# Optimization experiments

Hardware: AMD Instinct MI355X
Metric: run time of the kernel (lower is better)

## Reference

```python
import jax, jax.numpy as jnp
import numpy as np

B, C, H, W = 4, 64, 224, 224
WS = 14
HEADS = 4
HD = C // HEADS  # 16
N = WS * WS      # 196
SCALE = HD ** -0.5


def conv2d(x, w, b, pad):
    y = jax.lax.conv_general_dilated(x, w, (1, 1), [(pad, pad), (pad, pad)],
                                     dimension_numbers=('NCHW', 'OIHW', 'NCHW'))
    return y + b[None, :, None, None]


def layernorm(x, g, b, eps=1e-5):
    m = jnp.mean(x, axis=-1, keepdims=True)
    v = jnp.mean((x - m) ** 2, axis=-1, keepdims=True)
    return (x - m) * jax.lax.rsqrt(v + eps) * g + b


def window_partition(x):
    # x: (B,H,W,C) -> (B*nW, WS, WS, C)
    b, h, w, c = x.shape
    x = x.reshape(b, h // WS, WS, w // WS, WS, c)
    return x.transpose(0, 1, 3, 2, 4, 5).reshape(-1, WS, WS, c)


def window_reverse(win, h, w):
    b = win.shape[0] // ((h // WS) * (w // WS))
    x = win.reshape(b, h // WS, w // WS, WS, WS, -1)
    return x.transpose(0, 1, 3, 2, 4, 5).reshape(b, h, w, -1)


def setup_inputs():
    key = jax.random.key(0)
    ks = iter(jax.random.split(key, 64))
    nrm = lambda shp, s=0.02: (jax.random.normal(next(ks), shp, jnp.float32) * s)
    d = {}
    d['x'] = jax.random.normal(next(ks), (B, C, H, W), jnp.float32)
    d['x_basic'] = jax.random.normal(next(ks), (B, C, H, W), jnp.float32)
    # Aware_offset convs
    d['c1_w'] = nrm((64, 64, 3, 3)); d['c1_b'] = jnp.zeros((64,), jnp.float32)
    d['c2_w'] = nrm((64, 64, 5, 5)); d['c2_b'] = jnp.zeros((64,), jnp.float32)
    d['c3_w'] = nrm((64, 64, 7, 7)); d['c3_b'] = jnp.zeros((64,), jnp.float32)
    d['c4_w'] = nrm((64, 192, 3, 3)); d['c4_b'] = jnp.zeros((64,), jnp.float32)
    d['c5_w'] = nrm((128, 128, 3, 3)); d['c5_b'] = jnp.zeros((128,), jnp.float32)
    d['c6_w'] = nrm((128, 128, 3, 3)); d['c6_b'] = jnp.zeros((128,), jnp.float32)
    d['c7_w'] = nrm((64, 128, 1, 1)); d['c7_b'] = jnp.zeros((64,), jnp.float32)
    d['c8_w'] = nrm((64, 128, 1, 1)); d['c8_b'] = jnp.zeros((64,), jnp.float32)
    # block params
    d['qkv1_w'] = nrm((64, 64, 3, 3)); d['qkv1_b'] = jnp.zeros((64,), jnp.float32)
    d['n1_g'] = jnp.ones((C,), jnp.float32); d['n1_b'] = jnp.zeros((C,), jnp.float32)
    d['qkv_w'] = nrm((3 * C, C)); d['qkv_b'] = jnp.zeros((3 * C,), jnp.float32)
    d['corr_w'] = nrm((N, HD)); d['corr_b'] = jnp.zeros((N,), jnp.float32)
    d['proj_w'] = nrm((C, C)); d['proj_b'] = jnp.zeros((C,), jnp.float32)
    d['n2_g'] = jnp.ones((C,), jnp.float32); d['n2_b'] = jnp.zeros((C,), jnp.float32)
    d['fc1_w'] = nrm((2 * C, C)); d['fc1_b'] = jnp.zeros((2 * C,), jnp.float32)
    d['fc2_w'] = nrm((C, 2 * C)); d['fc2_b'] = jnp.zeros((C,), jnp.float32)
    return d


def _forward(x, x_basic, c1_w, c1_b, c2_w, c2_b, c3_w, c3_b, c4_w, c4_b,
             c5_w, c5_b, c6_w, c6_b, c7_w, c7_b, c8_w, c8_b,
             qkv1_w, qkv1_b, n1_g, n1_b, qkv_w, qkv_b, corr_w, corr_b,
             proj_w, proj_b, n2_g, n2_b, fc1_w, fc1_b, fc2_w, fc2_b):
    relu = jax.nn.relu
    # ---- Aware_offset ----
    in1 = relu(conv2d(x, c1_w, c1_b, 1))
    in2 = relu(conv2d(x, c2_w, c2_b, 2))
    in3 = relu(conv2d(x, c3_w, c3_b, 3))
    xo = relu(conv2d(jnp.concatenate([in1, in2, in3], 1), c4_w, c4_b, 1))
    cat12 = jnp.concatenate([x, x_basic], 1)
    b1 = relu(conv2d(cat12, c5_w, c5_b, 1))
    b2 = jax.nn.sigmoid(relu(conv2d(b1, c6_w, c6_b, 1)))
    b1 = relu(conv2d(b1 * b2, c7_w, c7_b, 0))
    xb = xo * b1 + relu(conv2d(cat12, c8_w, c8_b, 0))  # (B,C,H,W)
    xb = xb.transpose(0, 2, 3, 1)                       # (B,H,W,C)
    # ---- pre-attn: norm1 + convQKV1 ----
    xt = x.reshape(B, C, H * W).transpose(0, 2, 1)      # (B,L,C)
    xt = layernorm(xt, n1_g, n1_b)
    xc = xt.reshape(B, H, W, C).transpose(0, 3, 1, 2)
    xc = conv2d(xc, qkv1_w, qkv1_b, 1).transpose(0, 2, 3, 1)  # (B,H,W,C)
    # ---- windows ----
    xw = window_partition(xc).reshape(-1, N, C)   # (B_,N,C)
    xbw = window_partition(xb).reshape(-1, N, C)
    B_ = xw.shape[0]
    # ---- window attention with correction bias ----
    qkv = (xw @ qkv_w.T + qkv_b).reshape(B_, N, 3, HEADS, HD).transpose(2, 0, 3, 1, 4)
    q, k, v = qkv[0] * SCALE, qkv[1], qkv[2]            # (B_,h,N,hd)
    xcorr = xbw.reshape(B_, N, HEADS, HD).transpose(0, 2, 1, 3)
    xcorr = xcorr @ corr_w.T + corr_b                   # (B_,h,N,196)
    attn = jax.nn.softmax(jnp.einsum('bhnd,bhmd->bhnm', q, k) + xcorr, axis=-1)
    out = jnp.einsum('bhnm,bhmd->bhnd', attn, v).transpose(0, 2, 1, 3).reshape(B_, N, C)
    out = out @ proj_w.T + proj_b
    # ---- reverse + MLP ----
    sx = window_reverse(out.reshape(-1, WS, WS, C), H, W)  # (B,H,W,C)
    xt = sx.reshape(B, H * W, C)
    h = layernorm(xt, n2_g, n2_b)
    h = jax.nn.gelu(h @ fc1_w.T + fc1_b, approximate=False) @ fc2_w.T + fc2_b
    xt = xt + h
    return xt.reshape(B, H, W, C).transpose(0, 3, 1, 2)


def reference(x, x_basic, c1_w, c1_b, c2_w, c2_b, c3_w, c3_b, c4_w, c4_b,
              c5_w, c5_b, c6_w, c6_b, c7_w, c7_b, c8_w, c8_b,
              qkv1_w, qkv1_b, n1_g, n1_b, qkv_w, qkv_b, corr_w, corr_b,
              proj_w, proj_b, n2_g, n2_b, fc1_w, fc1_b, fc2_w, fc2_b):
    return _forward(x, x_basic, c1_w, c1_b, c2_w, c2_b, c3_w, c3_b, c4_w, c4_b,
                    c5_w, c5_b, c6_w, c6_b, c7_w, c7_b, c8_w, c8_b,
                    qkv1_w, qkv1_b, n1_g, n1_b, qkv_w, qkv_b, corr_w, corr_b,
                    proj_w, proj_b, n2_g, n2_b, fc1_w, fc1_b, fc2_w, fc2_b)
```

## Files before the change

### kernel.cpp

```cpp
#include <hip/hip_runtime.h>
#include <hip/hip_bf16.h>
#include <math.h>


#define HW  50176
#define WID 224

typedef unsigned short ushortT;
typedef __attribute__((ext_vector_type(8))) short bf8_t;
typedef __attribute__((ext_vector_type(4))) short bf4_t;
typedef __attribute__((ext_vector_type(4))) float f4_t;

__device__ __forceinline__ ushortT f2bf(float v) {
    __hip_bfloat16 h = __float2bfloat16(v);
    ushortT u; __builtin_memcpy(&u, &h, 2); return u;
}
__device__ __forceinline__ float bf2f(ushortT h) {
    union { float f; unsigned int u; } c; c.u = ((unsigned int)h) << 16;
    return c.f;
}
__device__ __forceinline__ void cvt8(const float* xv, bf8_t& hh, bf8_t& ll) {
    #pragma unroll
    for (int i = 0; i < 8; ++i) {
        ushortT hi = f2bf(xv[i]);
        hh[i] = (short)hi;
        ll[i] = (short)f2bf(xv[i] - bf2f(hi));
    }
}

__global__ __launch_bounds__(256) void packw(
    const float* __restrict__ w, ushortT* __restrict__ dst,
    int K, int IC, int OC, int total)
{
    int e = blockIdx.x * 256 + threadIdx.x;
    if (e >= total) return;
    int KK = K * K;
    int kk = e % KK; int rem = e / KK;
    int ic = rem % IC; int oc = rem / IC;
    float v = w[e];
    ushortT hi = f2bf(v);
    ushortT lo = f2bf(v - bf2f(hi));
    int g = oc >> 6, oc64 = oc & 63;
    int ic32 = ic >> 5, icin = ic & 31, kb = icin >> 3, ii = icin & 7;
    int nch = KK * (IC / 32);
    int chunk = ic32 * KK + kk;
    size_t base = ((size_t)(g * nch + chunk)) * 4096;
    dst[base + (kb * 64 + oc64) * 8 + ii] = hi;
    dst[base + 2048 + (kb * 64 + oc64) * 8 + ii] = lo;
}

__global__ __launch_bounds__(256) void packa32(
    const float* __restrict__ w, ushortT* __restrict__ dst, int K, int total)
{
    int e = blockIdx.x * 256 + threadIdx.x;
    if (e >= total) return;
    int f = e >> 9, r = e & 511, ln = r >> 3, i = r & 7;
    int nk = K >> 5;
    int o = f / nk, ks = f % nk;
    int c = ln & 15, gg = ln >> 4;
    float v = w[(size_t)(o * 16 + c) * K + ks * 32 + gg * 8 + i];
    ushortT hi = f2bf(v);
    dst[(size_t)f * 1024 + ln * 8 + i] = hi;
    dst[(size_t)f * 1024 + 512 + ln * 8 + i] = f2bf(v - bf2f(hi));
}

__global__ __launch_bounds__(256) void packa16(
    const float* __restrict__ w, ushortT* __restrict__ dst, int K, int total)
{
    int e = blockIdx.x * 256 + threadIdx.x;
    if (e >= total) return;
    int f = e >> 8, r = e & 255, ln = r >> 2, i = r & 3;
    int nk = K >> 4;
    int o = f / nk, n = f % nk;
    int c = ln & 15, gg = ln >> 4;
    float v = w[(size_t)(o * 16 + c) * K + n * 16 + gg * 4 + i];
    ushortT hi = f2bf(v);
    dst[(size_t)f * 512 + ln * 4 + i] = hi;
    dst[(size_t)f * 512 + 256 + ln * 4 + i] = f2bf(v - bf2f(hi));
}

template<int K>
__device__ __forceinline__ void convpass(
    const ushortT* __restrict__ wq, const ushortT* __restrict__ sm,
    int wv, int lc, int kb, f4_t (&ac)[2][4])
{
    constexpr int off = 3 - K / 2;
    constexpr int INSH = 14 * 22 * 40;
    constexpr int KK = K * K;
    const int boff = (kb * 64 + lc) * 8;

    bf8_t bA[4], lA[4], bB[4], lB[4];
    #pragma unroll
    for (int n = 0; n < 4; ++n) {
        bA[n] = *(const bf8_t*)(wq + boff + n * 128);
        lA[n] = *(const bf8_t*)(wq + 2048 + boff + n * 128);
    }
    auto domfma = [&](int kk, bf8_t (&bh)[4], bf8_t (&bl)[4]) {
        const int ky = kk / K, kx = kk % K;
        #pragma unroll
        for (int m = 0; m < 2; ++m) {
            const int row = 2 * wv + m + ky + off;
            const int col = lc + kx + off;
            const ushortT* ab = sm + (row * 22 + col) * 40 + kb * 8;
            bf8_t Ah = *(const bf8_t*)ab;
            bf8_t Al = *(const bf8_t*)(ab + INSH);
            #pragma unroll
            for (int n = 0; n < 4; ++n) {
                ac[m][n] = __builtin_amdgcn_mfma_f32_16x16x32_bf16(Ah, bh[n], ac[m][n], 0, 0, 0);
                ac[m][n] = __builtin_amdgcn_mfma_f32_16x16x32_bf16(Ah, bl[n], ac[m][n], 0, 0, 0);
                ac[m][n] = __builtin_amdgcn_mfma_f32_16x16x32_bf16(Al, bh[n], ac[m][n], 0, 0, 0);
            }
        }
    };
    #pragma unroll 1
    for (int kk = 0; kk + 2 <= KK; kk += 2) {
        const ushortT* w1 = wq + (size_t)(kk + 1) * 4096;
        #pragma unroll
        for (int n = 0; n < 4; ++n) {
            bB[n] = *(const bf8_t*)(w1 + boff + n * 128);
            lB[n] = *(const bf8_t*)(w1 + 2048 + boff + n * 128);
        }
        domfma(kk, bA, lA);
        const ushortT* w2 = wq + (size_t)(kk + 2) * 4096;
        #pragma unroll
        for (int n = 0; n < 4; ++n) {
            bA[n] = *(const bf8_t*)(w2 + boff + n * 128);
            lA[n] = *(const bf8_t*)(w2 + 2048 + boff + n * 128);
        }
        domfma(kk + 1, bB, lB);
    }
    domfma(KK - 1, bA, lA);
}

__global__ __launch_bounds__(256, 4) void mfconv3(
    const float* __restrict__ in,
    const ushortT* __restrict__ w1p, const ushortT* __restrict__ w2p,
    const ushortT* __restrict__ w3p,
    const float* __restrict__ b1, const float* __restrict__ b2,
    const float* __restrict__ b3,
    float* __restrict__ out, int inStride, int outStride)
{
    constexpr int TWd = 22, THd = 14, ICP = 40;
    constexpr int INSH = THd * TWd * ICP;
    constexpr int E = THd * TWd * 32;
    __shared__ __align__(16) ushortT smem_u[2 * INSH];

    const int t = threadIdx.x, lane = t & 63, wv = t >> 6;
    const int lc = lane & 15, kb = lane >> 4;
    const int img = blockIdx.z;
    const int x0 = blockIdx.x * 16, y0 = blockIdx.y * 8;
    const float* inb = in + (size_t)img * inStride;

    f4_t acc1[2][4], acc2[2][4], acc3[2][4];
    {
        #pragma unroll
        for (int n = 0; n < 4; ++n) {
            float z1 = b1[n * 16 + lc], z2 = b2[n * 16 + lc], z3 = b3[n * 16 + lc];
            #pragma unroll
            for (int m = 0; m < 2; ++m) {
                acc1[m][n] = (f4_t){z1, z1, z1, z1};
                acc2[m][n] = (f4_t){z2, z2, z2, z2};
                acc3[m][n] = (f4_t){z3, z3, z3, z3};
            }
        }
    }

    #pragma unroll 1
    for (int ic32 = 0; ic32 < 2; ++ic32) {
        __syncthreads();
        #pragma unroll 1
        for (int ib = 0; ib < E; ib += 2048) {
            float v[8];
            #pragma unroll
            for (int u = 0; u < 8; ++u) {
                int i = ib + u * 256 + t;
                v[u] = 0.f;
                if (i < E) {
                    int icn = i / (THd * TWd);
                    int px  = i % (THd * TWd);
                    int ty = px / TWd, tx = px % TWd;
                    int gy = y0 + ty - 3, gx = x0 + tx - 3;
                    if (gy >= 0 && gy < WID && gx >= 0 && gx < WID)
                        v[u] = inb[(size_t)(ic32 * 32 + icn) * HW + gy * WID + gx];
                }
            }
            #pragma unroll
            for (int u = 0; u < 8; ++u) {
                int i = ib + u * 256 + t;
                if (i < E) {
                    int icn = i / (THd * TWd);
                    int px  = i % (THd * TWd);
                    ushortT hi = f2bf(v[u]);
                    smem_u[px * ICP + icn] = hi;
                    smem_u[INSH + px * ICP + icn] = f2bf(v[u] - bf2f(hi));
                }
            }
        }
        __syncthreads();
        convpass<3>(w1p + (size_t)(ic32 *  9) * 4096, smem_u, wv, lc, kb, acc1);
        convpass<5>(w2p + (size_t)(ic32 * 25) * 4096, smem_u, wv, lc, kb, acc2);
        convpass<7>(w3p + (size_t)(ic32 * 49) * 4096, smem_u, wv, lc, kb, acc3);
    }

    #pragma unroll
    for (int c = 0; c < 3; ++c) {
        float* ob0 = out + (size_t)img * outStride + (size_t)(c * 64) * HW;
        #pragma unroll
        for (int m = 0; m < 2; ++m) {
            const int y = y0 + 2 * wv + m;
            #pragma unroll
            for (int n = 0; n < 4; ++n) {
                f4_t v = (c == 0) ? acc1[m][n] : (c == 1) ? acc2[m][n] : acc3[m][n];
                float4 st = { fmaxf(v[0], 0.f), fmaxf(v[1], 0.f),
                              fmaxf(v[2], 0.f), fmaxf(v[3], 0.f) };
                *(float4*)&ob0[(size_t)(n * 16 + lc) * HW + (size_t)y * WID + x0 + kb * 4] = st;
            }
        }
    }
}

template<int K, int IC, int OC, int ACT, bool CAT, bool LNRM, bool NHWCOUT>
__global__ __launch_bounds__(256, 4) void mfconv(
    const float* __restrict__ in, const float* __restrict__ in2,
    const ushortT* __restrict__ wpk, const float* __restrict__ bias,
    const float* __restrict__ mu, const float* __restrict__ rs,
    const float* __restrict__ lng, const float* __restrict__ lnb,
    float* __restrict__ out, int inStride, int outStride)
{
    constexpr int P = K / 2, TWd = 16 + K - 1, THd = 8 + K - 1, ICP = 40;
    constexpr int OCG = OC / 64, KK = K * K, NCH = KK * (IC / 32);
    constexpr int INSH = THd * TWd * ICP;
    constexpr int E = THd * TWd * 32;
    constexpr int SMU = (2 * INSH > 10240) ? 2 * INSH : 10240;
    __shared__ __align__(16) ushortT smem_u[SMU];
    float* pool = (float*)smem_u;

    const int t = threadIdx.x, lane = t & 63, wv = t >> 6;
    const int lc = lane & 15, kb = lane >> 4;
    const int img = blockIdx.z / OCG, g = blockIdx.z % OCG;
    const int x0 = blockIdx.x * 16, y0 = blockIdx.y * 8;
    const float* inb  = in + (size_t)img * inStride;
    const float* in2b = CAT ? (in2 + (size_t)img * inStride) : nullptr;
    const int imgPixBase = img * HW;
    const ushortT* wq0 = wpk + (size_t)g * NCH * 4096;

    f4_t acc[2][4];
    {
        float bz0 = bias[g * 64 +  0 + lc];
        float bz1 = bias[g * 64 + 16 + lc];
        float bz2 = bias[g * 64 + 32 + lc];
        float bz3 = bias[g * 64 + 48 + lc];
        #pragma unroll
        for (int m = 0; m < 2; ++m) {
            acc[m][0] = (f4_t){bz0, bz0, bz0, bz0};
            acc[m][1] = (f4_t){bz1, bz1, bz1, bz1};
            acc[m][2] = (f4_t){bz2, bz2, bz2, bz2};
            acc[m][3] = (f4_t){bz3, bz3, bz3, bz3};
        }
    }
    const int aoff = lc * ICP + kb * 8;
    const int boff = (kb * 64 + lc) * 8;

    #pragma unroll 1
    for (int ic32 = 0; ic32 < IC / 32; ++ic32) {
        __syncthreads();
        #pragma unroll 1
        for (int ib = 0; ib < E; ib += 2048) {
            float v[8];
            #pragma unroll
            for (int u = 0; u < 8; ++u) {
                int i = ib + u * 256 + t;
                v[u] = 0.f;
                if (i < E) {
                    int icn = i / (THd * TWd);
                    int px  = i % (THd * TWd);
                    int ty = px / TWd, tx = px % TWd;
                    int gy = y0 + ty - P, gx = x0 + tx - P;
                    int ic = ic32 * 32 + icn;
                    if (gy >= 0 && gy < WID && gx >= 0 && gx < WID) {
                        const float* s;
                        if (CAT) s = (ic < 64) ? (inb + (size_t)ic * HW)
                                               : (in2b + (size_t)(ic - 64) * HW);
                        else     s = inb + (size_t)ic * HW;
                        float vv = s[gy * WID + gx];
                        if (LNRM) {
                            int p = imgPixBase + gy * WID + gx;
                            vv = (vv - mu[p]) * rs[p] * lng[ic] + lnb[ic];
                        }
                        v[u] = vv;
                    }
                }
            }
            #pragma unroll
            for (int u = 0; u < 8; ++u) {
                int i = ib + u * 256 + t;
                if (i < E) {
                    int icn = i / (THd * TWd);
                    int px  = i % (THd * TWd);
                    ushortT hi = f2bf(v[u]);
                    smem_u[px * ICP + icn] = hi;
                    smem_u[INSH + px * ICP + icn] = f2bf(v[u] - bf2f(hi));
                }
            }
        }
        __syncthreads();
        const ushortT* wqb = wq0 + (size_t)(ic32 * KK) * 4096;
        bf8_t bA[4], lA[4], bB[4], lB[4];
        #pragma unroll
        for (int n = 0; n < 4; ++n) {
            bA[n] = *(const bf8_t*)(wqb + boff + n * 128);
            lA[n] = *(const bf8_t*)(wqb + 2048 + boff + n * 128);
        }
        auto domfma = [&](int kk, bf8_t (&bh)[4], bf8_t (&bl)[4]) {
            const int ky = kk / K, kx = kk % K;
            #pragma unroll
            for (int m = 0; m < 2; ++m) {
                const int row = 2 * wv + m + ky;
                const ushortT* ab = smem_u + (row * TWd + kx) * ICP + aoff;
                bf8_t Ah = *(const bf8_t*)ab;
                bf8_t Al = *(const bf8_t*)(ab + INSH);
                #pragma unroll
                for (int n = 0; n < 4; ++n) {
                    acc[m][n] = __builtin_amdgcn_mfma_f32_16x16x32_bf16(Ah, bh[n], acc[m][n], 0, 0, 0);
                    acc[m][n] = __builtin_amdgcn_mfma_f32_16x16x32_bf16(Ah, bl[n], acc[m][n], 0, 0, 0);
                    acc[m][n] = __builtin_amdgcn_mfma_f32_16x16x32_bf16(Al, bh[n], acc[m][n], 0, 0, 0);
                }
            }
        };
        #pragma unroll 1
        for (int kk = 0; kk + 2 <= KK; kk += 2) {
            const ushortT* w1 = wqb + (size_t)(kk + 1) * 4096;
            #pragma unroll
            for (int n = 0; n < 4; ++n) {
                bB[n] = *(const bf8_t*)(w1 + boff + n * 128);
                lB[n] = *(const bf8_t*)(w1 + 2048 + boff + n * 128);
            }
            domfma(kk, bA, lA);
            const ushortT* w2 = wqb + (size_t)(kk + 2) * 4096;
            #pragma unroll
            for (int n = 0; n < 4; ++n) {
                bA[n] = *(const bf8_t*)(w2 + boff + n * 128);
                lA[n] = *(const bf8_t*)(w2 + 2048 + boff + n * 128);
            }
            domfma(kk + 1, bB, lB);
        }
        domfma(KK - 1, bA, lA);
    }
    if (NHWCOUT) {
        float* ob0 = out + (size_t)img * outStride;
        #pragma unroll
        for (int m = 0; m < 2; ++m) {
            __syncthreads();
            #pragma unroll
            for (int n = 0; n < 4; ++n)
                #pragma unroll
                for (int j = 0; j < 4; ++j) {
                    float v = acc[m][n][j];
                    if (ACT == 1) v = fmaxf(v, 0.f);
                    else if (ACT == 2) v = 1.f / (1.f + __expf(-fmaxf(v, 0.f)));
                    pool[(wv * 16 + kb * 4 + j) * 68 + n * 16 + lc] = v;
                }
            __syncthreads();
            {
                int pix = t >> 2, q = t & 3;
                int y = y0 + 2 * (pix >> 4) + m;
                int x = x0 + (pix & 15);
                float* pr = ob0 + ((size_t)y * WID + x) * 64 + q * 16;
                const float* src = &pool[pix * 68 + q * 16];
                #pragma unroll
                for (int u = 0; u < 4; ++u)
                    *(float4*)&pr[u * 4] = *(const float4*)&src[u * 4];
            }
        }
    } else {
        float* ob0 = out + (size_t)img * outStride + (size_t)(g * 64) * HW;
        #pragma unroll
        for (int m = 0; m < 2; ++m) {
            const int y = y0 + 2 * wv + m;
            #pragma unroll
            for (int n = 0; n < 4; ++n) {
                f4_t v = acc[m][n];
                float4 st;
                #pragma unroll
                for (int j = 0; j < 4; ++j) {
                    float vv = v[j];
                    if (ACT == 1) vv = fmaxf(vv, 0.f);
                    else if (ACT == 2) vv = 1.f / (1.f + __expf(-fmaxf(vv, 0.f)));
                    ((float*)&st)[j] = vv;
                }
                *(float4*)&ob0[(size_t)(n * 16 + lc) * HW + (size_t)y * WID + x0 + kb * 4] = st;
            }
        }
    }
}

__global__ __launch_bounds__(256) void ln_stats(
    const float* __restrict__ x, float* __restrict__ mu, float* __restrict__ rs)
{
    const int p = blockIdx.x * 256 + threadIdx.x;
    const int img = p / HW, pp = p - img * HW;
    const float* b = x + (size_t)img * 64 * HW + pp;
    float row[64];
    #pragma unroll
    for (int c = 0; c < 64; ++c) row[c] = b[(size_t)c * HW];
    float s1 = 0.f;
    #pragma unroll
    for (int c = 0; c < 64; ++c) s1 += row[c];
    float m = s1 * (1.f / 64.f);
    float s2 = 0.f;
    #pragma unroll
    for (int c = 0; c < 64; ++c) { float d = row[c] - m; s2 += d * d; }
    mu[p] = m;
    rs[p] = rsqrtf(s2 * (1.f / 64.f) + 1e-5f);
}

__global__ __launch_bounds__(256) void xb1x1(
    const float* __restrict__ x, const float* __restrict__ xbas,
    const float* __restrict__ xo, const float* __restrict__ b1, const float* __restrict__ b2,
    const float* __restrict__ c7w, const float* __restrict__ c7b,
    const float* __restrict__ c8w, const float* __restrict__ c8b,
    float* __restrict__ xbout)
{
    __shared__ __align__(16) float w7s[128 * 36], w8s[128 * 36];
    const int t = threadIdx.x, oh = blockIdx.y;
    for (int i = t; i < 4096; i += 256) {
        int o = i >> 7, ic = i & 127;
        w7s[ic * 36 + o] = c7w[(size_t)(oh * 32 + o) * 128 + ic];
        w8s[ic * 36 + o] = c8w[(size_t)(oh * 32 + o) * 128 + ic];
    }
    __syncthreads();
    const int p = blockIdx.x * 256 + t;
    const int img = p / HW, pp = p - img * HW;
    const float* b1p = b1 + (size_t)img * 128 * HW + pp;
    const float* b2p = b2 + (size_t)img * 128 * HW + pp;
    const float* xp  = x  + (size_t)img * 64 * HW + pp;
    const float* xbp = xbas + (size_t)img * 64 * HW + pp;
    float a7[32], a8[32];
    {
        const float4* c74 = (const float4*)(c7b + oh * 32);
        const float4* c84 = (const float4*)(c8b + oh * 32);
        #pragma unroll
        for (int j4 = 0; j4 < 8; ++j4) {
            float4 v7 = c74[j4], v8 = c84[j4];
            a7[j4*4+0]=v7.x; a7[j4*4+1]=v7.y; a7[j4*4+2]=v7.z; a7[j4*4+3]=v7.w;
            a8[j4*4+0]=v8.x; a8[j4*4+1]=v8.y; a8[j4*4+2]=v8.z; a8[j4*4+3]=v8.w;
        }
    }
    #pragma unroll 4
    for (int ic = 0; ic < 128; ++ic) {
        float tv = b1p[(size_t)ic * HW] * b2p[(size_t)ic * HW];
        float cv = (ic < 64) ? xp[(size_t)ic * HW] : xbp[(size_t)(ic - 64) * HW];
        const float4* w7r = (const float4*)&w7s[ic * 36];
        const float4* w8r = (const float4*)&w8s[ic * 36];
        #pragma unroll
        for (int j4 = 0; j4 < 8; ++j4) {
            float4 v7 = w7r[j4], v8 = w8r[j4];
            a7[j4*4+0] = fmaf(tv, v7.x, a7[j4*4+0]);
            a7[j4*4+1] = fmaf(tv, v7.y, a7[j4*4+1]);
            a7[j4*4+2] = fmaf(tv, v7.z, a7[j4*4+2]);
            a7[j4*4+3] = fmaf(tv, v7.w, a7[j4*4+3]);
            a8[j4*4+0] = fmaf(cv, v8.x, a8[j4*4+0]);
            a8[j4*4+1] = fmaf(cv, v8.y, a8[j4*4+1]);
            a8[j4*4+2] = fmaf(cv, v8.z, a8[j4*4+2]);
            a8[j4*4+3] = fmaf(cv, v8.w, a8[j4*4+3]);
        }
    }
    const float* xop = xo + (size_t)img * 64 * HW + pp;
    float* orow = xbout + (size_t)p * 64 + oh * 32;
    #pragma unroll
    for (int j4 = 0; j4 < 8; ++j4) {
        float4 st;
        st.x = xop[(size_t)(oh*32 + j4*4+0) * HW] * fmaxf(a7[j4*4+0], 0.f) + fmaxf(a8[j4*4+0], 0.f);
        st.y = xop[(size_t)(oh*32 + j4*4+1) * HW] * fmaxf(a7[j4*4+1], 0.f) + fmaxf(a8[j4*4+1], 0.f);
        st.z = xop[(size_t)(oh*32 + j4*4+2) * HW] * fmaxf(a7[j4*4+2], 0.f) + fmaxf(a8[j4*4+2], 0.f);
        st.w = xop[(size_t)(oh*32 + j4*4+3) * HW] * fmaxf(a7[j4*4+3], 0.f) + fmaxf(a8[j4*4+3], 0.f);
        *(float4*)&orow[j4 * 4] = st;
    }
}

__global__ __launch_bounds__(256) void attn(
    const float* __restrict__ xc, const float* __restrict__ xb,
    const float* __restrict__ qkvw, const float* __restrict__ qkvb,
    const float* __restrict__ corw, const float* __restrict__ corb,
    float* __restrict__ aout)
{
    constexpr int QS = 40;
    constexpr int VS = 212;
    __shared__ __align__(16) ushortT Kth[196 * QS];
    __shared__ __align__(16) ushortT Ktl[196 * QS];
    __shared__ __align__(16) ushortT Vth[16 * VS];
    __shared__ __align__(16) ushortT Vtl[16 * VS];
    __shared__ __align__(16) float CB[208];

    const int t = threadIdx.x;
    const int wdw = blockIdx.x >> 2, h = blockIdx.x & 3;
    const int b = wdw >> 8, wl = wdw & 255;
    const int wy = (wl >> 4) * 14, wx = (wl & 15) * 14;
    const int lane = t & 63, wv = t >> 6;
    const int g = lane >> 4, col = lane & 15;

    bf8_t Wqh[2], Wql[2], Wkh[2], Wkl[2], Wvh[2], Wvl[2];
    float qb[4], kb[4], vb[4];
    {
        #pragma unroll
        for (int ks = 0; ks < 2; ++ks) {
            float xv[8];
            const float* wr = qkvw + (h * 16 + col) * 64 + ks * 32 + g * 8;
            *(float4*)&xv[0] = *(const float4*)wr;
            *(float4*)&xv[4] = *(const float4*)(wr + 4);
            cvt8(xv, Wqh[ks], Wql[ks]);
            wr = qkvw + (64 + h * 16 + col) * 64 + ks * 32 + g * 8;
            *(float4*)&xv[0] = *(const float4*)wr;
            *(float4*)&xv[4] = *(const float4*)(wr + 4);
            cvt8(xv, Wkh[ks], Wkl[ks]);
            wr = qkvw + (128 + h * 16 + col) * 64 + ks * 32 + g * 8;
            *(float4*)&xv[0] = *(const float4*)wr;
            *(float4*)&xv[4] = *(const float4*)(wr + 4);
            cvt8(xv, Wvh[ks], Wvl[ks]);
        }
        float4 q4 = *(const float4*)(qkvb + h * 16 + g * 4);
        float4 k4 = *(const float4*)(qkvb + 64 + h * 16 + g * 4);
        float4 v4 = *(const float4*)(qkvb + 128 + h * 16 + g * 4);
        qb[0]=q4.x; qb[1]=q4.y; qb[2]=q4.z; qb[3]=q4.w;
        kb[0]=k4.x; kb[1]=k4.y; kb[2]=k4.z; kb[3]=k4.w;
        vb[0]=v4.x; vb[1]=v4.y; vb[2]=v4.z; vb[3]=v4.w;
    }

    if (t < 208) CB[t] = (t < 196) ? corb[t] : 0.f;
    if (t < 196) {
        unsigned* khr = (unsigned*)&Kth[t * QS];
        unsigned* klr = (unsigned*)&Ktl[t * QS];
        float xw[16];
        const float4* cw4 = (const float4*)(corw + t * 16);
        #pragma unroll
        for (int j = 0; j < 4; ++j) *(float4*)&xw[j * 4] = cw4[j];
        #pragma unroll
        for (int i = 0; i < 8; ++i) {
            ushortT ah = f2bf(xw[2*i]), bh = f2bf(xw[2*i+1]);
            ushortT al = f2bf(xw[2*i] - bf2f(ah)), bl = f2bf(xw[2*i+1] - bf2f(bh));
            khr[8 + i] = (unsigned)ah | ((unsigned)bh << 16);
            klr[8 + i] = (unsigned)al | ((unsigned)bl << 16);
        }
    }

    auto phaseB = [&](int mt) -> f4_t {
        const int row = 16 * mt + col;
        const int pix = (row > 195) ? 195 : row;
        const int rr = pix / 14, cc = pix - (pix / 14) * 14;
        const float* xr = xc + (size_t)((b * 224 + wy + rr) * 224 + wx + cc) * 64;
        f4_t dq = (f4_t){0.f, 0.f, 0.f, 0.f};
        f4_t dk = (f4_t){0.f, 0.f, 0.f, 0.f};
        f4_t dv = (f4_t){0.f, 0.f, 0.f, 0.f};
        #pragma unroll
        for (int ks = 0; ks < 2; ++ks) {
            float xv[8];
            *(float4*)&xv[0] = *(const float4*)(xr + ks * 32 + g * 8);
            *(float4*)&xv[4] = *(const float4*)(xr + ks * 32 + g * 8 + 4);
            bf8_t Xh, Xl;
            cvt8(xv, Xh, Xl);
            dq = __builtin_amdgcn_mfma_f32_16x16x32_bf16(Wqh[ks], Xh, dq, 0, 0, 0);
            dq = __builtin_amdgcn_mfma_f32_16x16x32_bf16(Wqh[ks], Xl, dq, 0, 0, 0);
            dq = __builtin_amdgcn_mfma_f32_16x16x32_bf16(Wql[ks], Xh, dq, 0, 0, 0);
            dk = __builtin_amdgcn_mfma_f32_16x16x32_bf16(Wkh[ks], Xh, dk, 0, 0, 0);
            dk = __builtin_amdgcn_mfma_f32_16x16x32_bf16(Wkh[ks], Xl, dk, 0, 0, 0);
            dk = __builtin_amdgcn_mfma_f32_16x16x32_bf16(Wkl[ks], Xh, dk, 0, 0, 0);
            dv = __builtin_amdgcn_mfma_f32_16x16x32_bf16(Wvh[ks], Xh, dv, 0, 0, 0);
            dv = __builtin_amdgcn_mfma_f32_16x16x32_bf16(Wvh[ks], Xl, dv, 0, 0, 0);
            dv = __builtin_amdgcn_mfma_f32_16x16x32_bf16(Wvl[ks], Xh, dv, 0, 0, 0);
        }
        #pragma unroll
        for (int j = 0; j < 4; ++j) {
            float v = dv[j] + vb[j];
            ushortT hi = f2bf(v);
            Vth[(g * 4 + j) * VS + row] = hi;
            Vtl[(g * 4 + j) * VS + row] = f2bf(v - bf2f(hi));
        }
        if (row < 196) {
            unsigned h0, h1, l0, l1;
            {
                float a = dk[0] + kb[0], bb = dk[1] + kb[1];
                ushortT ah = f2bf(a), bh = f2bf(bb);
                h0 = (unsigned)ah | ((unsigned)bh << 16);
                l0 = (unsigned)f2bf(a - bf2f(ah)) | ((unsigned)f2bf(bb - bf2f(bh)) << 16);
            }
            {
                float a = dk[2] + kb[2], bb = dk[3] + kb[3];
                ushortT ah = f2bf(a), bh = f2bf(bb);
                h1 = (unsigned)ah | ((unsigned)bh << 16);
                l1 = (unsigned)f2bf(a - bf2f(ah)) | ((unsigned)f2bf(bb - bf2f(bh)) << 16);
            }
            uint2 u;
            u.x = h0; u.y = h1; *(uint2*)&Kth[row * QS + g * 4] = u;
            u.x = l0; u.y = l1; *(uint2*)&Ktl[row * QS + g * 4] = u;
        }
        return (f4_t){(dq[0] + qb[0]) * 0.25f, (dq[1] + qb[1]) * 0.25f,
                      (dq[2] + qb[2]) * 0.25f, (dq[3] + qb[3]) * 0.25f};
    };

    f4_t dqs0 = phaseB(wv);
    f4_t dqs1 = phaseB(wv + 4);
    f4_t dqs2 = phaseB(wv + 8);
    f4_t dqs3 = (f4_t){0.f, 0.f, 0.f, 0.f};
    if (wv == 0) dqs3 = phaseB(12);
    __syncthreads();

    auto phaseC = [&](f4_t dqv, int qt) {
        const int row = 16 * qt + col;
        const int pixq = (row > 195) ? 195 : row;
        float q8[8];
        const int sl0 = ((2 * g) & 3) * 16 + col;
        const int sl1 = ((2 * g + 1) & 3) * 16 + col;
        q8[0] = __shfl(dqv[0], sl0); q8[1] = __shfl(dqv[1], sl0);
        q8[2] = __shfl(dqv[2], sl0); q8[3] = __shfl(dqv[3], sl0);
        q8[4] = __shfl(dqv[0], sl1); q8[5] = __shfl(dqv[1], sl1);
        q8[6] = __shfl(dqv[2], sl1); q8[7] = __shfl(dqv[3], sl1);
        if (g >= 2) {
            const int rr = pixq / 14, cc = pixq - (pixq / 14) * 14;
            const float* xr = xb + (size_t)((b * 224 + wy + rr) * 224 + wx + cc) * 64
                            + h * 16 + (g & 1) * 8;
            *(float4*)&q8[0] = *(const float4*)xr;
            *(float4*)&q8[4] = *(const float4*)(xr + 4);
        }
        bf8_t Bhf, Blf;
        cvt8(q8, Bhf, Blf);
        f4_t s[13];
        __builtin_amdgcn_s_setprio(1);
        #pragma unroll
        for (int kt = 0; kt < 13; ++kt) {
            const int krow = (16 * kt + col > 195) ? 195 : (16 * kt + col);
            const bf8_t Ahf = *(const bf8_t*)&Kth[krow * QS + g * 8];
            const bf8_t Alf = *(const bf8_t*)&Ktl[krow * QS + g * 8];
            f4_t a = (f4_t){0.f, 0.f, 0.f, 0.f};
            a = __builtin_amdgcn_mfma_f32_16x16x32_bf16(Ahf, Bhf, a, 0, 0, 0);
            a = __builtin_amdgcn_mfma_f32_16x16x32_bf16(Ahf, Blf, a, 0, 0, 0);
            a = __builtin_amdgcn_mfma_f32_16x16x32_bf16(Alf, Bhf, a, 0, 0, 0);
            const f4_t cb4 = *(const f4_t*)&CB[16 * kt + g * 4];
            s[kt] = a + cb4;
        }
        __builtin_amdgcn_s_setprio(0);
        if (g > 0) { s[12][0] = -3e38f; s[12][1] = -3e38f; s[12][2] = -3e38f; s[12][3] = -3e38f; }
        float mrow = -3e38f;
        #pragma unroll
        for (int kt = 0; kt < 13; ++kt)
            #pragma unroll
            for (int j = 0; j < 4; ++j) mrow = fmaxf(mrow, s[kt][j]);
        mrow = fmaxf(mrow, __shfl_xor(mrow, 16));
        mrow = fmaxf(mrow, __shfl_xor(mrow, 32));
        float lsum = 0.f;
        bf4_t ph[13], pl[13];
        #pragma unroll
        for (int kt = 0; kt < 13; ++kt) {
            #pragma unroll
            for (int j = 0; j < 4; ++j) {
                float p = __expf(s[kt][j] - mrow);
                lsum += p;
                ushortT hi = f2bf(p);
                ph[kt][j] = (short)hi;
                pl[kt][j] = (short)f2bf(p - bf2f(hi));
            }
        }
        lsum += __shfl_xor(lsum, 16);
        lsum += __shfl_xor(lsum, 32);
        f4_t o = (f4_t){0.f, 0.f, 0.f, 0.f};
        __builtin_amdgcn_s_setprio(1);
        #pragma unroll
        for (int kt = 0; kt < 13; ++kt) {
            const bf4_t vh = *(const bf4_t*)&Vth[col * VS + 16 * kt + g * 4];
            const bf4_t vl = *(const bf4_t*)&Vtl[col * VS + 16 * kt + g * 4];
            o = __builtin_amdgcn_mfma_f32_16x16x16bf16_1k(vh, ph[kt], o, 0, 0, 0);
            o = __builtin_amdgcn_mfma_f32_16x16x16bf16_1k(vl, ph[kt], o, 0, 0, 0);
            o = __builtin_amdgcn_mfma_f32_16x16x16bf16_1k(vh, pl[kt], o, 0, 0, 0);
        }
        __builtin_amdgcn_s_setprio(0);
        const int pix = 16 * qt + col;
        if (pix < 196) {
            const float inv = 1.f / lsum;
            const int rr = pix / 14, cc = pix % 14;
            const size_t pixIdx = (size_t)((b * 224 + wy + rr) * 224 + wx + cc);
            float4 st = { o[0] * inv, o[1] * inv, o[2] * inv, o[3] * inv };
            *(float4*)&aout[pixIdx * 64 + h * 16 + g * 4] = st;
        }
    };

    phaseC(dqs0, wv);
    phaseC(dqs1, wv + 4);
    phaseC(dqs2, wv + 8);
    if (wv == 0) phaseC(dqs3, 12);
}

__global__ __launch_bounds__(256) void mlpmf(
    const float* __restrict__ aout, const ushortT* __restrict__ pk,
    const float* __restrict__ pbias,
    const float* __restrict__ lng, const float* __restrict__ lnb,
    const float* __restrict__ fc1b, const float* __restrict__ fc2b,
    float* __restrict__ out)
{
    const int t = threadIdx.x, lane = t & 63, wv = t >> 6;
    const int gq = lane >> 4, col = lane & 15;
    const int p0 = (blockIdx.x * 4 + wv) * 16;
    const ushortT* pk1 = pk;
    const ushortT* pk2 = pk + 8192;
    const ushortT* pk3 = pk + 24576;

    f4_t S[4];
    #pragma unroll
    for (int n = 0; n < 4; ++n) {
        float4 b4 = *(const float4*)(pbias + n * 16 + gq * 4);
        S[n] = (f4_t){b4.x, b4.y, b4.z, b4.w};
    }
    const float* xr = aout + (size_t)(p0 + col) * 64;
    #pragma unroll
    for (int ks = 0; ks < 2; ++ks) {
        float xv[8];
        *(float4*)&xv[0] = *(const float4*)(xr + ks * 32 + gq * 8);
        *(float4*)&xv[4] = *(const float4*)(xr + ks * 32 + gq * 8 + 4);
        bf8_t Xh, Xl;
        cvt8(xv, Xh, Xl);
        #pragma unroll
        for (int n = 0; n < 4; ++n) {
            const ushortT* a = pk1 + (size_t)(n * 2 + ks) * 1024 + lane * 8;
            bf8_t Ah = *(const bf8_t*)a;
            bf8_t Al = *(const bf8_t*)(a + 512);
            S[n] = __builtin_amdgcn_mfma_f32_16x16x32_bf16(Ah, Xh, S[n], 0, 0, 0);
            S[n] = __builtin_amdgcn_mfma_f32_16x16x32_bf16(Ah, Xl, S[n], 0, 0, 0);
            S[n] = __builtin_amdgcn_mfma_f32_16x16x32_bf16(Al, Xh, S[n], 0, 0, 0);
        }
    }
    float sum = 0.f;
    #pragma unroll
    for (int n = 0; n < 4; ++n)
        #pragma unroll
        for (int j = 0; j < 4; ++j) sum += S[n][j];
    sum += __shfl_xor(sum, 16);
    sum += __shfl_xor(sum, 32);
    float mean = sum * (1.f / 64.f);
    float var = 0.f;
    #pragma unroll
    for (int n = 0; n < 4; ++n)
        #pragma unroll
        for (int j = 0; j < 4; ++j) { float d = S[n][j] - mean; var += d * d; }
    var += __shfl_xor(var, 16);
    var += __shfl_xor(var, 32);
    float rstd = rsqrtf(var * (1.f / 64.f) + 1e-5f);
    bf4_t Nh[4], Nl[4];
    #pragma unroll
    for (int n = 0; n < 4; ++n) {
        float4 g4 = *(const float4*)(lng + n * 16 + gq * 4);
        float4 b4 = *(const float4*)(lnb + n * 16 + gq * 4);
        float nv0 = (S[n][0] - mean) * rstd * g4.x + b4.x;
        float nv1 = (S[n][1] - mean) * rstd * g4.y + b4.y;
        float nv2 = (S[n][2] - mean) * rstd * g4.z + b4.z;
        float nv3 = (S[n][3] - mean) * rstd * g4.w + b4.w;
        ushortT h0 = f2bf(nv0), h1 = f2bf(nv1), h2 = f2bf(nv2), h3 = f2bf(nv3);
        Nh[n][0] = (short)h0; Nh[n][1] = (short)h1; Nh[n][2] = (short)h2; Nh[n][3] = (short)h3;
        Nl[n][0] = (short)f2bf(nv0 - bf2f(h0));
        Nl[n][1] = (short)f2bf(nv1 - bf2f(h1));
        Nl[n][2] = (short)f2bf(nv2 - bf2f(h2));
        Nl[n][3] = (short)f2bf(nv3 - bf2f(h3));
    }
    bf4_t Gh[8], Gl[8];
    #pragma unroll
    for (int o = 0; o < 8; ++o) {
        float4 b4 = *(const float4*)(fc1b + o * 16 + gq * 4);
        f4_t hacc = (f4_t){b4.x, b4.y, b4.z, b4.w};
        #pragma unroll
        for (int n = 0; n < 4; ++n) {
            const ushortT* a = pk2 + (size_t)(o * 4 + n) * 512 + lane * 4;
            bf4_t Ah = *(const bf4_t*)a;
            bf4_t Al = *(const bf4_t*)(a + 256);
            hacc = __builtin_amdgcn_mfma_f32_16x16x16bf16_1k(Ah, Nh[n], hacc, 0, 0, 0);
            hacc = __builtin_amdgcn_mfma_f32_16x16x16bf16_1k(Ah, Nl[n], hacc, 0, 0, 0);
            hacc = __builtin_amdgcn_mfma_f32_16x16x16bf16_1k(Al, Nh[n], hacc, 0, 0, 0);
        }
        #pragma unroll
        for (int j = 0; j < 4; ++j) {
            float hv = hacc[j];
            float gl = 0.5f * hv * (1.f + erff(hv * 0.70710678118f));
            ushortT hi = f2bf(gl);
            Gh[o][j] = (short)hi;
            Gl[o][j] = (short)f2bf(gl - bf2f(hi));
        }
    }
    const int img = p0 / HW, pp = p0 - img * HW;
    float* ob = out + (size_t)img * 64 * HW + pp + col;
    #pragma unroll
    for (int o2 = 0; o2 < 4; ++o2) {
        float4 b4 = *(const float4*)(fc2b + o2 * 16 + gq * 4);
        f4_t oacc = (f4_t){b4.x, b4.y, b4.z, b4.w};
        #pragma unroll
        for (int k2 = 0; k2 < 8; ++k2) {
            const ushortT* a = pk3 + (size_t)(o2 * 8 + k2) * 512 + lane * 4;
            bf4_t Ah = *(const bf4_t*)a;
            bf4_t Al = *(const bf4_t*)(a + 256);
            oacc = __builtin_amdgcn_mfma_f32_16x16x16bf16_1k(Ah, Gh[k2], oacc, 0, 0, 0);
            oacc = __builtin_amdgcn_mfma_f32_16x16x16bf16_1k(Ah, Gl[k2], oacc, 0, 0, 0);
            oacc = __builtin_amdgcn_mfma_f32_16x16x16bf16_1k(Al, Gh[k2], oacc, 0, 0, 0);
        }
        #pragma unroll
        for (int j = 0; j < 4; ++j) {
            int och = o2 * 16 + gq * 4 + j;
            ob[(size_t)och * HW] = S[o2][j] + oacc[j];
        }
    }
}

extern "C" void kernel_launch(void* const* d_in, const int* in_sizes, int n_in,
                              void* d_out, int out_size, void* d_ws, size_t ws_size,
                              hipStream_t stream)
{
    (void)in_sizes; (void)n_in; (void)out_size;
    const float* x      = (const float*)d_in[0];
    const float* xbasic = (const float*)d_in[1];
    const float* c1w  = (const float*)d_in[2];  const float* c1b  = (const float*)d_in[3];
    const float* c2w  = (const float*)d_in[4];  const float* c2b  = (const float*)d_in[5];
    const float* c3w  = (const float*)d_in[6];  const float* c3b  = (const float*)d_in[7];
    const float* c4w  = (const float*)d_in[8];  const float* c4b  = (const float*)d_in[9];
    const float* c5w  = (const float*)d_in[10]; const float* c5b  = (const float*)d_in[11];
    const float* c6w  = (const float*)d_in[12]; const float* c6b  = (const float*)d_in[13];
    const float* c7w  = (const float*)d_in[14]; const float* c7b  = (const float*)d_in[15];
    const float* c8w  = (const float*)d_in[16]; const float* c8b  = (const float*)d_in[17];
    const float* qk1w = (const float*)d_in[18]; const float* qk1b = (const float*)d_in[19];
    const float* n1g  = (const float*)d_in[20]; const float* n1b  = (const float*)d_in[21];
    const float* qkvw = (const float*)d_in[22]; const float* qkvb = (const float*)d_in[23];
    const float* corw = (const float*)d_in[24]; const float* corb = (const float*)d_in[25];
    const float* prjw = (const float*)d_in[26]; const float* prjb = (const float*)d_in[27];
    const float* n2g  = (const float*)d_in[28]; const float* n2b  = (const float*)d_in[29];
    const float* f1w  = (const float*)d_in[30]; const float* f1b  = (const float*)d_in[31];
    const float* f2w  = (const float*)d_in[32]; const float* f2b  = (const float*)d_in[33];

    float* ws = (float*)d_ws;
    const size_t SCR0 = 26836992ull;
    const size_t need4 = (SCR0 + 4ull * 19267584ull) * 4ull;
    const size_t need2 = (SCR0 + 2ull * 19267584ull) * 4ull;
    const int CS = (ws_size >= need4) ? 4 : (ws_size >= need2) ? 2 : 1;
    const int nch = 4 / CS;

    float* XC = ws;
    float* XB = ws + 12845056;
    float* MU = ws + 25690112;
    float* RS = ws + 25890816;
    ushortT* WP = (ushortT*)(ws + 26091520);
    float* A  = ws + SCR0;
    float* XO = A + (size_t)CS * 9633792;
    float* B1 = XO + (size_t)CS * 3211264;
    float* B2 = A;
    float* AOUT = A;
    ushortT* WQ1 = (ushortT*)B1;
    ushortT* PM  = (ushortT*)MU;

    const size_t o1 = 0, o2 = 73728, o3 = 278528, o4 = 679936, o5 = 901120, o6 = 1196032;

    ln_stats<<<784, 256, 0, stream>>>(x, MU, RS);

    {
        auto PK = [&](const float* w, ushortT* dst, int K, int IC, int OC) {
            int tot = OC * IC * K * K;
            packw<<<(tot + 255) / 256, 256, 0, stream>>>(w, dst, K, IC, OC, tot);
        };
        PK(qk1w, WQ1, 3, 64, 64);
        PK(c1w, WP + o1, 3, 64, 64);
        PK(c2w, WP + o2, 5, 64, 64);
        PK(c3w, WP + o3, 7, 64, 64);
        PK(c4w, WP + o4, 3, 192, 64);
        PK(c5w, WP + o5, 3, 128, 128);
        PK(c6w, WP + o6, 3, 128, 128);
    }

    mfconv<3, 64, 64, 0, false, true, true><<<dim3(14, 28, 4), 256, 0, stream>>>(
        x, nullptr, WQ1, qk1b, MU, RS, n1g, n1b, XC, 64 * HW, HW * 64);

    packa32<<<16, 256, 0, stream>>>(prjw, PM, 64, 4096);
    packa16<<<32, 256, 0, stream>>>(f1w, PM + 8192, 64, 8192);
    packa16<<<32, 256, 0, stream>>>(f2w, PM + 24576, 128, 8192);

    for (int ch = 0; ch < nch; ++ch) {
        const float* xi  = x      + (size_t)ch * CS * 64 * HW;
        const float* xbi = xbasic + (size_t)ch * CS * 64 * HW;
        mfconv3<<<dim3(14, 28, CS), 256, 0, stream>>>(
            xi, WP + o1, WP + o2, WP + o3, c1b, c2b, c3b, A, 64 * HW, 192 * HW);
        mfconv<3, 192, 64, 1, false, false, false><<<dim3(14, 28, CS), 256, 0, stream>>>(
            A, nullptr, WP + o4, c4b, nullptr, nullptr, nullptr, nullptr, XO, 192 * HW, 64 * HW);
        mfconv<3, 128, 128, 1, true, false, false><<<dim3(14, 28, CS * 2), 256, 0, stream>>>(
            xi, xbi, WP + o5, c5b, nullptr, nullptr, nullptr, nullptr, B1, 64 * HW, 128 * HW);
        mfconv<3, 128, 128, 2, false, false, false><<<dim3(14, 28, CS * 2), 256, 0, stream>>>(
            B1, nullptr, WP + o6, c6b, nullptr, nullptr, nullptr, nullptr, B2, 128 * HW, 128 * HW);
        xb1x1<<<dim3(CS * 196, 2), 256, 0, stream>>>(
            xi, xbi, XO, B1, B2, c7w, c7b, c8w, c8b, XB + (size_t)ch * CS * HW * 64);
    }

    attn<<<4096, 256, 0, stream>>>(XC, XB, qkvw, qkvb, corw, corb, AOUT);
    mlpmf<<<3136, 256, 0, stream>>>(AOUT, PM, prjb, n2g, n2b, f1b, f2b,
                                    (float*)d_out);
}
```

Before: 1.656 ms.

## Switch multi-scale conv kernel to 32x32x16 MFMA with repacked weights

Rewrites the fused 3x3/5x5/7x7 conv kernel to use 32x32x16 bf16 MFMA instructions instead of 16x16x32. Weights get a new packing layout matched to the 32-wide operand, and the accumulator layout and output stores are remapped. The larger MFMA is meant to raise operand reuse and reduce the instruction and LDS-read count per FLOP. In exchange the 16-wide accumulators raise register pressure, so occupancy is lowered from 4 to 3 blocks per SM via launch bounds.

```diff
diff --git a/kernel.cpp b/kernel.cpp
--- a/kernel.cpp
+++ b/kernel.cpp
@@ -10,6 +10,7 @@
 typedef __attribute__((ext_vector_type(8))) short bf8_t;
 typedef __attribute__((ext_vector_type(4))) short bf4_t;
 typedef __attribute__((ext_vector_type(4))) float f4_t;
+typedef __attribute__((ext_vector_type(16))) float f16v;
 
 __device__ __forceinline__ ushortT f2bf(float v) {
     __hip_bfloat16 h = __float2bfloat16(v);
@@ -49,6 +50,27 @@
     dst[base + 2048 + (kb * 64 + oc64) * 8 + ii] = lo;
 }
 
+__global__ __launch_bounds__(256) void packw32(
+    const float* __restrict__ w, ushortT* __restrict__ dst,
+    int K, int total)
+{
+    int e = blockIdx.x * 256 + threadIdx.x;
+    if (e >= total) return;
+    int KK = K * K;
+    int kk = e % KK; int rem = e / KK;
+    int ic = rem & 63; int oc = rem >> 6;
+    float v = w[e];
+    ushortT hi = f2bf(v);
+    ushortT lo = f2bf(v - bf2f(hi));
+    int ic32 = ic >> 5, icin = ic & 31;
+    int ks = icin >> 4, kloc = icin & 15, khalf = kloc >> 3, i = kloc & 7;
+    int oct = oc >> 5;
+    int lane = khalf * 32 + (oc & 31);
+    size_t f = ((size_t)(ic32 * KK + kk) * 2 + ks) * 2 + oct;
+    dst[f * 1024 + lane * 8 + i] = hi;
+    dst[f * 1024 + 512 + lane * 8 + i] = lo;
+}
+
 __global__ __launch_bounds__(256) void packa32(
     const float* __restrict__ w, ushortT* __restrict__ dst, int K, int total)
 {
@@ -80,59 +102,54 @@
 }
 
 template<int K>
-__device__ __forceinline__ void convpass(
+__device__ __forceinline__ void convpass32(
     const ushortT* __restrict__ wq, const ushortT* __restrict__ sm,
-    int wv, int lc, int kb, f4_t (&ac)[2][4])
+    int wv, int lane, f16v (&ac)[2])
 {
     constexpr int off = 3 - K / 2;
     constexpr int INSH = 14 * 22 * 40;
     constexpr int KK = K * K;
-    const int boff = (kb * 64 + lc) * 8;
-
-    bf8_t bA[4], lA[4], bB[4], lB[4];
-    #pragma unroll
-    for (int n = 0; n < 4; ++n) {
-        bA[n] = *(const bf8_t*)(wq + boff + n * 128);
-        lA[n] = *(const bf8_t*)(wq + 2048 + boff + n * 128);
-    }
-    auto domfma = [&](int kk, bf8_t (&bh)[4], bf8_t (&bl)[4]) {
+    const int xin = lane & 15, ysub = (lane >> 4) & 1, khalf = lane >> 5;
+    const int boff = lane * 8;
+
+    bf8_t hA[2], lA[2], hB[2], lB[2];
+    auto loadstep = [&](int s, bf8_t (&h)[2], bf8_t (&l)[2]) {
+        const ushortT* base = wq + (size_t)(s >> 1) * 4096 + (size_t)(s & 1) * 2048;
+        #pragma unroll
+        for (int oct = 0; oct < 2; ++oct) {
+            h[oct] = *(const bf8_t*)(base + oct * 1024 + boff);
+            l[oct] = *(const bf8_t*)(base + oct * 1024 + 512 + boff);
+        }
+    };
+    auto dostep = [&](int s, bf8_t (&h)[2], bf8_t (&l)[2]) {
+        const int kk = s >> 1, ks = s & 1;
         const int ky = kk / K, kx = kk % K;
-        #pragma unroll
-        for (int m = 0; m < 2; ++m) {
-            const int row = 2 * wv + m + ky + off;
-            const int col = lc + kx + off;
-            const ushortT* ab = sm + (row * 22 + col) * 40 + kb * 8;
-            bf8_t Ah = *(const bf8_t*)ab;
-            bf8_t Al = *(const bf8_t*)(ab + INSH);
-            #pragma unroll
-            for (int n = 0; n < 4; ++n) {
-                ac[m][n] = __builtin_amdgcn_mfma_f32_16x16x32_bf16(Ah, bh[n], ac[m][n], 0, 0, 0);
-                ac[m][n] = __builtin_amdgcn_mfma_f32_16x16x32_bf16(Ah, bl[n], ac[m][n], 0, 0, 0);
-                ac[m][n] = __builtin_amdgcn_mfma_f32_16x16x32_bf16(Al, bh[n], ac[m][n], 0, 0, 0);
-            }
+        const int row = 2 * wv + ysub + ky + off;
+        const int col = xin + kx + off;
+        const ushortT* ab = sm + (row * 22 + col) * 40 + ks * 16 + khalf * 8;
+        bf8_t Ah = *(const bf8_t*)ab;
+        bf8_t Al = *(const bf8_t*)(ab + INSH);
+        #pragma unroll
+        for (int oct = 0; oct < 2; ++oct) {
+            ac[oct] = __builtin_amdgcn_mfma_f32_32x32x16_bf16(Ah, h[oct], ac[oct], 0, 0, 0);
+            ac[oct] = __builtin_amdgcn_mfma_f32_32x32x16_bf16(Ah, l[oct], ac[oct], 0, 0, 0);
+            ac[oct] = __builtin_amdgcn_mfma_f32_32x32x16_bf16(Al, h[oct], ac[oct], 0, 0, 0);
         }
     };
+    loadstep(0, hA, lA);
     #pragma unroll 1
-    for (int kk = 0; kk + 2 <= KK; kk += 2) {
-        const ushortT* w1 = wq + (size_t)(kk + 1) * 4096;
-        #pragma unroll
-        for (int n = 0; n < 4; ++n) {
-            bB[n] = *(const bf8_t*)(w1 + boff + n * 128);
-            lB[n] = *(const bf8_t*)(w1 + 2048 + boff + n * 128);
-        }
-        domfma(kk, bA, lA);
-        const ushortT* w2 = wq + (size_t)(kk + 2) * 4096;
-        #pragma unroll
-        for (int n = 0; n < 4; ++n) {
-            bA[n] = *(const bf8_t*)(w2 + boff + n * 128);
-            lA[n] = *(const bf8_t*)(w2 + 2048 + boff + n * 128);
-        }
-        domfma(kk + 1, bB, lB);
-    }
-    domfma(KK - 1, bA, lA);
-}
-
-__global__ __launch_bounds__(256, 4) void mfconv3(
+    for (int s = 0; s < 2 * KK - 2; s += 2) {
+        loadstep(s + 1, hB, lB);
+        dostep(s, hA, lA);
+        loadstep(s + 2, hA, lA);
+        dostep(s + 1, hB, lB);
+    }
+    loadstep(2 * KK - 1, hB, lB);
+    dostep(2 * KK - 2, hA, lA);
+    dostep(2 * KK - 1, hB, lB);
+}
+
+__global__ __launch_bounds__(256, 3) void mfconv3(
     const float* __restrict__ in,
     const ushortT* __restrict__ w1p, const ushortT* __restrict__ w2p,
     const ushortT* __restrict__ w3p,
@@ -146,22 +163,19 @@
     __shared__ __align__(16) ushortT smem_u[2 * INSH];
 
     const int t = threadIdx.x, lane = t & 63, wv = t >> 6;
-    const int lc = lane & 15, kb = lane >> 4;
+    const int khalf = lane >> 5;
     const int img = blockIdx.z;
     const int x0 = blockIdx.x * 16, y0 = blockIdx.y * 8;
     const float* inb = in + (size_t)img * inStride;
 
-    f4_t acc1[2][4], acc2[2][4], acc3[2][4];
-    {
-        #pragma unroll
-        for (int n = 0; n < 4; ++n) {
-            float z1 = b1[n * 16 + lc], z2 = b2[n * 16 + lc], z3 = b3[n * 16 + lc];
-            #pragma unroll
-            for (int m = 0; m < 2; ++m) {
-                acc1[m][n] = (f4_t){z1, z1, z1, z1};
-                acc2[m][n] = (f4_t){z2, z2, z2, z2};
-                acc3[m][n] = (f4_t){z3, z3, z3, z3};
-            }
+    f16v acc1[2], acc2[2], acc3[2];
+    #pragma unroll
+    for (int oct = 0; oct < 2; ++oct) {
+        const int oc = oct * 32 + (lane & 31);
+        float z1 = b1[oc], z2 = b2[oc], z3 = b3[oc];
+        #pragma unroll
+        for (int i = 0; i < 16; ++i) {
+            acc1[oct][i] = z1; acc2[oct][i] = z2; acc3[oct][i] = z3;
         }
     }
 
@@ -197,23 +211,26 @@
             }
         }
         __syncthreads();
-        convpass<3>(w1p + (size_t)(ic32 *  9) * 4096, smem_u, wv, lc, kb, acc1);
-        convpass<5>(w2p + (size_t)(ic32 * 25) * 4096, smem_u, wv, lc, kb, acc2);
-        convpass<7>(w3p + (size_t)(ic32 * 49) * 4096, smem_u, wv, lc, kb, acc3);
+        convpass32<3>(w1p + (size_t)(ic32 *  9) * 4096, smem_u, wv, lane, acc1);
+        convpass32<5>(w2p + (size_t)(ic32 * 25) * 4096, smem_u, wv, lane, acc2);
+        convpass32<7>(w3p + (size_t)(ic32 * 49) * 4096, smem_u, wv, lane, acc3);
     }
 
     #pragma unroll
     for (int c = 0; c < 3; ++c) {
         float* ob0 = out + (size_t)img * outStride + (size_t)(c * 64) * HW;
         #pragma unroll
-        for (int m = 0; m < 2; ++m) {
-            const int y = y0 + 2 * wv + m;
-            #pragma unroll
-            for (int n = 0; n < 4; ++n) {
-                f4_t v = (c == 0) ? acc1[m][n] : (c == 1) ? acc2[m][n] : acc3[m][n];
-                float4 st = { fmaxf(v[0], 0.f), fmaxf(v[1], 0.f),
-                              fmaxf(v[2], 0.f), fmaxf(v[3], 0.f) };
-                *(float4*)&ob0[(size_t)(n * 16 + lc) * HW + (size_t)y * WID + x0 + kb * 4] = st;
+        for (int oct = 0; oct < 2; ++oct) {
+            const int oc = oct * 32 + (lane & 31);
+            f16v a = (c == 0) ? acc1[oct] : (c == 1) ? acc2[oct] : acc3[oct];
+            #pragma unroll
+            for (int q = 0; q < 4; ++q) {
+                const int pb = 8 * q + 4 * khalf;
+                const int xb = pb & 15;
+                const int y  = y0 + 2 * wv + (pb >> 4);
+                float4 st = { fmaxf(a[4*q+0], 0.f), fmaxf(a[4*q+1], 0.f),
+                              fmaxf(a[4*q+2], 0.f), fmaxf(a[4*q+3], 0.f) };
+                *(float4*)&ob0[(size_t)oc * HW + (size_t)y * WID + x0 + xb] = st;
             }
         }
     }
@@ -857,10 +874,14 @@
             int tot = OC * IC * K * K;
             packw<<<(tot + 255) / 256, 256, 0, stream>>>(w, dst, K, IC, OC, tot);
         };
+        auto PK32 = [&](const float* w, ushortT* dst, int K) {
+            int tot = 4096 * K * K;
+            packw32<<<(tot + 255) / 256, 256, 0, stream>>>(w, dst, K, tot);
+        };
         PK(qk1w, WQ1, 3, 64, 64);
-        PK(c1w, WP + o1, 3, 64, 64);
-        PK(c2w, WP + o2, 5, 64, 64);
-        PK(c3w, WP + o3, 7, 64, 64);
+        PK32(c1w, WP + o1, 3);
+        PK32(c2w, WP + o2, 5);
+        PK32(c3w, WP + o3, 7);
         PK(c4w, WP + o4, 3, 192, 64);
         PK(c5w, WP + o5, 3, 128, 128);
         PK(c6w, WP + o6, 3, 128, 128);
```

New measurement: 1.931 ms. +16.6%, slower.

## Prefetch next input-channel chunk into registers during MFMA conv pass

Applied to the files above, without the earlier changes.

Both conv kernels now load the next 32-channel input tile from global memory into registers before running the MFMA passes on the current tile, then write it to shared memory after a barrier. This hides global load latency behind compute instead of serialising load, convert and compute. The cost is more registers per thread (NB*8 floats, up to 5 chunks for the 7x7 tile), which under launch_bounds(256,4) may cause spills or lower occupancy.

```diff
diff --git a/kernel.cpp b/kernel.cpp
--- a/kernel.cpp
+++ b/kernel.cpp
@@ -143,6 +143,7 @@
     constexpr int TWd = 22, THd = 14, ICP = 40;
     constexpr int INSH = THd * TWd * ICP;
     constexpr int E = THd * TWd * 32;
+    constexpr int NB = (E + 2047) / 2048;
     __shared__ __align__(16) ushortT smem_u[2 * INSH];
 
     const int t = threadIdx.x, lane = t & 63, wv = t >> 6;
@@ -165,42 +166,53 @@
         }
     }
 
-    #pragma unroll 1
-    for (int ic32 = 0; ic32 < 2; ++ic32) {
-        __syncthreads();
-        #pragma unroll 1
-        for (int ib = 0; ib < E; ib += 2048) {
-            float v[8];
+    float vreg[NB][8];
+    auto loadChunk = [&](int ic32) {
+        #pragma unroll
+        for (int b = 0; b < NB; ++b)
             #pragma unroll
             for (int u = 0; u < 8; ++u) {
-                int i = ib + u * 256 + t;
-                v[u] = 0.f;
+                int i = b * 2048 + u * 256 + t;
+                vreg[b][u] = 0.f;
                 if (i < E) {
                     int icn = i / (THd * TWd);
                     int px  = i % (THd * TWd);
                     int ty = px / TWd, tx = px % TWd;
                     int gy = y0 + ty - 3, gx = x0 + tx - 3;
                     if (gy >= 0 && gy < WID && gx >= 0 && gx < WID)
-                        v[u] = inb[(size_t)(ic32 * 32 + icn) * HW + gy * WID + gx];
+                        vreg[b][u] = inb[(size_t)(ic32 * 32 + icn) * HW + gy * WID + gx];
                 }
             }
+    };
+    auto writeChunk = [&]() {
+        #pragma unroll
+        for (int b = 0; b < NB; ++b)
             #pragma unroll
             for (int u = 0; u < 8; ++u) {
-                int i = ib + u * 256 + t;
+                int i = b * 2048 + u * 256 + t;
                 if (i < E) {
                     int icn = i / (THd * TWd);
                     int px  = i % (THd * TWd);
-                    ushortT hi = f2bf(v[u]);
+                    ushortT hi = f2bf(vreg[b][u]);
                     smem_u[px * ICP + icn] = hi;
-                    smem_u[INSH + px * ICP + icn] = f2bf(v[u] - bf2f(hi));
+                    smem_u[INSH + px * ICP + icn] = f2bf(vreg[b][u] - bf2f(hi));
                 }
             }
-        }
-        __syncthreads();
-        convpass<3>(w1p + (size_t)(ic32 *  9) * 4096, smem_u, wv, lc, kb, acc1);
-        convpass<5>(w2p + (size_t)(ic32 * 25) * 4096, smem_u, wv, lc, kb, acc2);
-        convpass<7>(w3p + (size_t)(ic32 * 49) * 4096, smem_u, wv, lc, kb, acc3);
-    }
+    };
+
+    loadChunk(0);
+    writeChunk();
+    __syncthreads();
+    loadChunk(1);
+    convpass<3>(w1p, smem_u, wv, lc, kb, acc1);
+    convpass<5>(w2p, smem_u, wv, lc, kb, acc2);
+    convpass<7>(w3p, smem_u, wv, lc, kb, acc3);
+    __syncthreads();
+    writeChunk();
+    __syncthreads();
+    convpass<3>(w1p + (size_t) 9 * 4096, smem_u, wv, lc, kb, acc1);
+    convpass<5>(w2p + (size_t)25 * 4096, smem_u, wv, lc, kb, acc2);
+    convpass<7>(w3p + (size_t)49 * 4096, smem_u, wv, lc, kb, acc3);
 
     #pragma unroll
     for (int c = 0; c < 3; ++c) {
@@ -229,8 +241,10 @@
 {
     constexpr int P = K / 2, TWd = 16 + K - 1, THd = 8 + K - 1, ICP = 40;
     constexpr int OCG = OC / 64, KK = K * K, NCH = KK * (IC / 32);
+    constexpr int NC = IC / 32;
     constexpr int INSH = THd * TWd * ICP;
     constexpr int E = THd * TWd * 32;
+    constexpr int NB = (E + 2047) / 2048;
     constexpr int SMU = (2 * INSH > 10240) ? 2 * INSH : 10240;
     __shared__ __align__(16) ushortT smem_u[SMU];
     float* pool = (float*)smem_u;
@@ -261,16 +275,14 @@
     const int aoff = lc * ICP + kb * 8;
     const int boff = (kb * 64 + lc) * 8;
 
-    #pragma unroll 1
-    for (int ic32 = 0; ic32 < IC / 32; ++ic32) {
-        __syncthreads();
-        #pragma unroll 1
-        for (int ib = 0; ib < E; ib += 2048) {
-            float v[8];
+    float vreg[NB][8];
+    auto loadChunk = [&](int ic32) {
+        #pragma unroll
+        for (int b = 0; b < NB; ++b)
             #pragma unroll
             for (int u = 0; u < 8; ++u) {
-                int i = ib + u * 256 + t;
-                v[u] = 0.f;
+                int i = b * 2048 + u * 256 + t;
+                vreg[b][u] = 0.f;
                 if (i < E) {
                     int icn = i / (THd * TWd);
                     int px  = i % (THd * TWd);
@@ -287,23 +299,33 @@
                             int p = imgPixBase + gy * WID + gx;
                             vv = (vv - mu[p]) * rs[p] * lng[ic] + lnb[ic];
                         }
-                        v[u] = vv;
+                        vreg[b][u] = vv;
                     }
                 }
             }
+    };
+    auto writeChunk = [&]() {
+        #pragma unroll
+        for (int b = 0; b < NB; ++b)
             #pragma unroll
             for (int u = 0; u < 8; ++u) {
-                int i = ib + u * 256 + t;
+                int i = b * 2048 + u * 256 + t;
                 if (i < E) {
                     int icn = i / (THd * TWd);
                     int px  = i % (THd * TWd);
-                    ushortT hi = f2bf(v[u]);
+                    ushortT hi = f2bf(vreg[b][u]);
                     smem_u[px * ICP + icn] = hi;
-                    smem_u[INSH + px * ICP + icn] = f2bf(v[u] - bf2f(hi));
+                    smem_u[INSH + px * ICP + icn] = f2bf(vreg[b][u] - bf2f(hi));
                 }
             }
-        }
+    };
+
+    loadChunk(0);
+    #pragma unroll 1
+    for (int ic32 = 0; ic32 < NC; ++ic32) {
+        writeChunk();
         __syncthreads();
+        if (ic32 + 1 < NC) loadChunk(ic32 + 1);
         const ushortT* wqb = wq0 + (size_t)(ic32 * KK) * 4096;
         bf8_t bA[4], lA[4], bB[4], lB[4];
         #pragma unroll
@@ -345,6 +367,7 @@
             domfma(kk + 1, bB, lB);
         }
         domfma(KK - 1, bA, lA);
+        __syncthreads();
     }
     if (NHWCOUT) {
         float* ob0 = out + (size_t)img * outStride;
```

After: 2.777 ms. 67.7% more time.
